# Kernel tuning notes

Measured on AMD Instinct MI355X. Metric: run time of the kernel, lower is better.

The kernel has to match this reference:

```python
import jax, jax.numpy as jnp
import numpy as np

EMBED, HIDDEN, VOCAB, FEAT_DIM = 256, 512, 10000, 1024
B, NREG, CAPLEN = 128, 49, 33


def setup_inputs() -> dict:
    key = jax.random.key(0)
    ks = jax.random.split(key, 20)
    xav = lambda k, shp: jax.random.uniform(k, shp, jnp.float32, -1.0, 1.0) * jnp.sqrt(6.0 / (shp[0] + shp[1]))
    d = {
        "features": jax.random.normal(ks[0], (B, NREG, FEAT_DIM), jnp.float32),
        "captions": jax.random.randint(ks[1], (B, CAPLEN), 0, VOCAB),
        "emb": jax.random.uniform(ks[2], (VOCAB, EMBED), jnp.float32, -0.1, 0.1),
        "W_ft": jax.random.uniform(ks[3], (EMBED, FEAT_DIM), jnp.float32, -0.1, 0.1),
        "b_ft": jnp.zeros((EMBED,), jnp.float32),
        "W_i": xav(ks[4], (2 * EMBED, HIDDEN)), "U_i": xav(ks[5], (HIDDEN, HIDDEN)), "b_i": jnp.zeros((HIDDEN,), jnp.float32),
        "W_f": xav(ks[6], (2 * EMBED, HIDDEN)), "U_f": xav(ks[7], (HIDDEN, HIDDEN)), "b_f": jnp.zeros((HIDDEN,), jnp.float32),
        "W_c": xav(ks[8], (2 * EMBED, HIDDEN)), "U_c": xav(ks[9], (HIDDEN, HIDDEN)), "b_c": jnp.zeros((HIDDEN,), jnp.float32),
        "W_o": xav(ks[10], (2 * EMBED, HIDDEN)), "U_o": xav(ks[11], (HIDDEN, HIDDEN)), "b_o": jnp.zeros((HIDDEN,), jnp.float32),
        "W_fc": jax.random.uniform(ks[12], (VOCAB, HIDDEN), jnp.float32, -0.1, 0.1),
        "b_fc": jnp.zeros((VOCAB,), jnp.float32),
    }
    return d


def reference(features, captions, emb, W_ft, b_ft,
              W_i, U_i, b_i, W_f, U_f, b_f, W_c, U_c, b_c, W_o, U_o, b_o,
              W_fc, b_fc):
    # mean-pool image regions, project to embed space
    feats_emb = features.mean(axis=1) @ W_ft.T + b_ft            # [B, E]
    embeds = emb[captions[:, :-1]]                                # [B, T, E]
    xs = jnp.swapaxes(embeds, 0, 1)                               # [T, B, E]

    h0 = jnp.zeros((features.shape[0], HIDDEN), features.dtype)
    c0 = jnp.zeros_like(h0)

    def step(carry, e_t):
        h, c = carry
        x = jnp.concatenate([e_t, feats_emb], axis=1)             # [B, 2E] (dropout=eval identity)
        i = jax.nn.sigmoid(x @ W_i + h @ U_i + b_i)
        f = jax.nn.sigmoid(x @ W_f + h @ U_f + b_f)
        g = jnp.tanh(x @ W_c + h @ U_c + b_c)
        o = jax.nn.sigmoid(x @ W_o + h @ U_o + b_o)
        c_new = f * c + i * g
        h_new = o * jnp.tanh(c_new)
        return (h_new, c_new), h_new

    _, hs = jax.lax.scan(step, (h0, c0), xs)                      # hs: [T, B, H]
    outputs = jnp.einsum('tbh,vh->btv', hs, W_fc) + b_fc          # [B, T, V]
    return outputs
```

## Files before the change

### kernel.cpp

```cpp
#include <hip/hip_runtime.h>
#include <hip/hip_bf16.h>

#define EMBED    256
#define HIDDEN   512
#define VOCAB    10000
#define WFC_PAD  10112
#define FEAT_DIM 1024
#define BATCH    128
#define NREGS    49
#define TSTEPS   32

typedef unsigned short u16;
typedef unsigned long long u64;
using f32x4 = __attribute__((ext_vector_type(4))) float;
using s16x8 = __attribute__((ext_vector_type(8))) short;
using u32x4 = __attribute__((ext_vector_type(4))) unsigned;

__device__ __forceinline__ u16 f2bf(float f) {
  __hip_bfloat16 h = __float2bfloat16(f);
  return *reinterpret_cast<u16*>(&h);
}
__device__ __forceinline__ float sig_(float x) {
  return 1.0f / (1.0f + __expf(-x));
}
__device__ __forceinline__ float tanh_(float x) {
  x = fminf(fmaxf(x, -15.f), 15.f);
  float e = __expf(2.f * x);
  return (e - 1.f) / (e + 1.f);
}
__device__ __forceinline__ void gl_lds16(const u16* g, u16* l) {
  __builtin_amdgcn_global_load_lds(
      (const __attribute__((address_space(1))) unsigned*)g,
      (__attribute__((address_space(3))) unsigned*)l, 16, 0, 0);
}

__global__ __launch_bounds__(256)
void k_feats(const float* __restrict__ features, const float* __restrict__ W_ft,
             const float* __restrict__ b_ft, float* __restrict__ feats_emb) {
  __shared__ float mean[FEAT_DIM];
  int b = blockIdx.x, tid = threadIdx.x;
  const float* fb = features + (size_t)b * NREGS * FEAT_DIM;
  for (int d = tid; d < FEAT_DIM; d += 256) {
    float s = 0.f;
    for (int r = 0; r < NREGS; ++r) s += fb[r * FEAT_DIM + d];
    mean[d] = s * (1.0f / 49.0f);
  }
  __syncthreads();
  const float* w = W_ft + (size_t)tid * FEAT_DIM;
  float acc = b_ft[tid];
#pragma unroll 4
  for (int d = 0; d < FEAT_DIM; d += 4) {
    float4 m4 = *(const float4*)&mean[d];
    float4 w4 = *(const float4*)&w[d];
    acc += m4.x * w4.x + m4.y * w4.y + m4.z * w4.z + m4.w * w4.w;
  }
  feats_emb[b * EMBED + tid] = acc;
}

struct GatePtrs {
  const float* W[4];
  const float* U[4];
  const float* b[4];
};

__global__ __launch_bounds__(256)
void k_transpose_wu(GatePtrs p, u16* __restrict__ WcatT, u16* __restrict__ UcatT) {
  __shared__ float tile[64][65];
  int g = blockIdx.y;
  const float* src = blockIdx.z ? p.U[g] : p.W[g];
  u16* dst = blockIdx.z ? UcatT : WcatT;
  int tj = (blockIdx.x & 7) * 64;
  int tk = (blockIdx.x >> 3) * 64;
  int tx = threadIdx.x & 63, ty = threadIdx.x >> 6;
#pragma unroll
  for (int i = 0; i < 16; ++i)
    tile[ty + 4 * i][tx] = src[(size_t)(tk + ty + 4 * i) * HIDDEN + tj + tx];
  __syncthreads();
#pragma unroll
  for (int i = 0; i < 16; ++i)
    dst[(size_t)(g * 512 + tj + ty + 4 * i) * 512 + tk + tx] = f2bf(tile[tx][ty + 4 * i]);
}

__global__ __launch_bounds__(256)
void k_prep2(GatePtrs p, const float* __restrict__ W_fc,
             float* __restrict__ bcat, u16* __restrict__ Wfc_bf) {
  int idx = blockIdx.x * 256 + threadIdx.x;
  if (idx < WFC_PAD * HIDDEN / 4) {
    size_t e0 = (size_t)idx * 4;
    ushort4 o;
    if (e0 < (size_t)VOCAB * HIDDEN) {
      float4 v = *(const float4*)(W_fc + e0);
      o.x = f2bf(v.x); o.y = f2bf(v.y); o.z = f2bf(v.z); o.w = f2bf(v.w);
    } else {
      o.x = o.y = o.z = o.w = 0;
    }
    *(ushort4*)(Wfc_bf + e0) = o;
  }
  if (idx < 4 * HIDDEN) bcat[idx] = p.b[idx >> 9][idx & 511];
}

__global__ __launch_bounds__(256)
void k_build_x(const float* __restrict__ emb, const int* __restrict__ captions,
               const float* __restrict__ feats_emb, u16* __restrict__ X) {
  int idx = blockIdx.x * 256 + threadIdx.x;
  int r = idx >> 9, col = idx & 511;
  int t = r >> 7, b = r & 127;
  float v;
  if (col < EMBED) {
    int tok = captions[b * 33 + t];
    v = emb[(size_t)tok * EMBED + col];
  } else {
    v = feats_emb[b * EMBED + (col - EMBED)];
  }
  X[idx] = f2bf(v);
}

__global__ __launch_bounds__(256)
void k_gemm_bt(const u16* __restrict__ A, const u16* __restrict__ Bt,
               const float* __restrict__ bias, float* __restrict__ C,
               int M, int N, int K, int out_mode) {
  __shared__ u16 Al[128 * 32];
  __shared__ u16 Bl[128 * 32];
  int tid = threadIdx.x;
  int lane = tid & 63;
  int w = tid >> 6;
  int wr = w & 1, wc = w >> 1;

  int Mtiles = gridDim.y, Ntiles = gridDim.x;
  int nwg = Mtiles * Ntiles;
  int id = blockIdx.y * Ntiles + blockIdx.x;
  int q = nwg >> 3, r = nwg & 7;
  int xcd = id & 7, pos = id >> 3;
  int wg = (xcd < r ? xcd * (q + 1) : r * (q + 1) + (xcd - r) * q) + pos;
  int m0 = (wg % Mtiles) * 128;
  int n0 = (wg / Mtiles) * 128;

  f32x4 acc[4][4];
#pragma unroll
  for (int i = 0; i < 4; ++i)
#pragma unroll
    for (int j = 0; j < 4; ++j) acc[i][j] = (f32x4){0.f, 0.f, 0.f, 0.f};

  int srowq = lane >> 2;
  int skq   = (lane & 3) * 8;

  for (int k0 = 0; k0 < K; k0 += 32) {
    __syncthreads();
#pragma unroll
    for (int i = 0; i < 2; ++i) {
      int rr = w * 32 + i * 16;
      gl_lds16(A + (size_t)(m0 + rr + srowq) * K + k0 + skq, Al + rr * 32);
      gl_lds16(Bt + (size_t)(n0 + rr + srowq) * K + k0 + skq, Bl + rr * 32);
    }
    __syncthreads();

    const u16* ab = Al + (wr * 64 + (lane & 15)) * 32 + (lane >> 4) * 8;
    const u16* bb = Bl + (wc * 64 + (lane & 15)) * 32 + (lane >> 4) * 8;
    s16x8 af[4], bf_[4];
#pragma unroll
    for (int mi = 0; mi < 4; ++mi) af[mi] = *(const s16x8*)(ab + mi * 16 * 32);
#pragma unroll
    for (int ni = 0; ni < 4; ++ni) bf_[ni] = *(const s16x8*)(bb + ni * 16 * 32);
#pragma unroll
    for (int mi = 0; mi < 4; ++mi)
#pragma unroll
      for (int ni = 0; ni < 4; ++ni)
        acc[mi][ni] = __builtin_amdgcn_mfma_f32_16x16x32_bf16(af[mi], bf_[ni], acc[mi][ni], 0, 0, 0);
  }

  int rbase = (lane >> 4) * 4;
  int colf = lane & 15;
#pragma unroll
  for (int mi = 0; mi < 4; ++mi) {
    int mbase = m0 + wr * 64 + mi * 16 + rbase;
#pragma unroll
    for (int ni = 0; ni < 4; ++ni) {
      int n = n0 + wc * 64 + ni * 16 + colf;
      if (n < N) {
        float bv = bias[n];
#pragma unroll
        for (int reg = 0; reg < 4; ++reg) {
          int mm = mbase + reg;
          float v = acc[mi][ni][reg] + bv;
          if (out_mode == 0) {
            C[(size_t)mm * N + n] = v;
          } else {
            C[(size_t)(mm & 127) * (TSTEPS * VOCAB) + (size_t)(mm >> 7) * VOCAB + n] = v;
          }
        }
      }
    }
  }
}

#define USTR 520

__global__ __launch_bounds__(256, 1)
void k_lstm_all(const u16* __restrict__ UcatT, const float* __restrict__ gates_pre,
                unsigned* __restrict__ hx, int* __restrict__ flags) {
  __shared__ u16 Ul[128 * USTR];
  int tid = threadIdx.x;
  int lane = tid & 63;
  int w = tid >> 6;
  int wr = w & 1, wj = w >> 1;
  int mg = blockIdx.x >> 4;
  int jb = blockIdx.x & 15;
  int b0 = mg * 32;
  int j0 = jb * 32;

  for (int i = tid; i < 128 * 64; i += 256) {
    int row = i >> 6;
    int kc = (i & 63) * 8;
    int gr = ((row >> 5) << 9) + j0 + (row & 31);
    uint4 v = *(const uint4*)(UcatT + (size_t)gr * 512 + kc);
    *(uint4*)(Ul + row * USTR + kc) = v;
  }
  __syncthreads();

  int jloc = wj * 16 + (lane & 15);
  int jj = j0 + jloc;
  int rb = wr * 16 + (lane >> 4) * 4;
  int arow = b0 + wr * 16 + (lane & 15);
  const u16* ubase = Ul + (size_t)jloc * USTR + (lane >> 4) * 8;
  int* myflag = flags + mg * 16 + jb;
  const int* pollp = flags + mg * 16 + (lane & 15);

  float c[4] = {0.f, 0.f, 0.f, 0.f};
  float gpv[16];

#pragma unroll
  for (int reg = 0; reg < 4; ++reg)
#pragma unroll
    for (int gi = 0; gi < 4; ++gi)
      gpv[reg * 4 + gi] = gates_pre[((size_t)(b0 + rb + reg)) * 2048 + gi * 512 + jj];

#pragma unroll 1
  for (int t = 0; t < TSTEPS; ++t) {
    f32x4 acc[4];
#pragma unroll
    for (int gi = 0; gi < 4; ++gi) acc[gi] = (f32x4){0.f, 0.f, 0.f, 0.f};

    if (t > 0) {
      int fv;
      do {
        asm volatile(
            "global_load_dword %0, %1, off sc0 sc1\n\t"
            "s_waitcnt vmcnt(0)"
            : "=v"(fv) : "v"(pollp) : "memory");
      } while (!__all(fv >= t));

      const u16* hp = (const u16*)hx + ((size_t)(t - 1) * 128 + arow) * 512 + (lane >> 4) * 8;
      u32x4 f[16];
      asm volatile(
          "global_load_dwordx4 %0, %4, off sc0 sc1\n\t"
          "global_load_dwordx4 %1, %4, off offset:64 sc0 sc1\n\t"
          "global_load_dwordx4 %2, %4, off offset:128 sc0 sc1\n\t"
          "global_load_dwordx4 %3, %4, off offset:192 sc0 sc1"
          : "=&v"(f[0]), "=&v"(f[1]), "=&v"(f[2]), "=&v"(f[3])
          : "v"(hp) : "memory");
      asm volatile(
          "global_load_dwordx4 %0, %4, off offset:256 sc0 sc1\n\t"
          "global_load_dwordx4 %1, %4, off offset:320 sc0 sc1\n\t"
          "global_load_dwordx4 %2, %4, off offset:384 sc0 sc1\n\t"
          "global_load_dwordx4 %3, %4, off offset:448 sc0 sc1"
          : "=&v"(f[4]), "=&v"(f[5]), "=&v"(f[6]), "=&v"(f[7])
          : "v"(hp) : "memory");
      asm volatile(
          "global_load_dwordx4 %0, %4, off offset:512 sc0 sc1\n\t"
          "global_load_dwordx4 %1, %4, off offset:576 sc0 sc1\n\t"
          "global_load_dwordx4 %2, %4, off offset:640 sc0 sc1\n\t"
          "global_load_dwordx4 %3, %4, off offset:704 sc0 sc1"
          : "=&v"(f[8]), "=&v"(f[9]), "=&v"(f[10]), "=&v"(f[11])
          : "v"(hp) : "memory");
      asm volatile(
          "global_load_dwordx4 %0, %4, off offset:768 sc0 sc1\n\t"
          "global_load_dwordx4 %1, %4, off offset:832 sc0 sc1\n\t"
          "global_load_dwordx4 %2, %4, off offset:896 sc0 sc1\n\t"
          "global_load_dwordx4 %3, %4, off offset:960 sc0 sc1\n\t"
          "s_waitcnt vmcnt(0)"
          : "=&v"(f[12]), "=&v"(f[13]), "=&v"(f[14]), "=&v"(f[15])
          : "v"(hp) : "memory");
      __builtin_amdgcn_sched_barrier(0);

#pragma unroll
      for (int kk = 0; kk < 16; ++kk) {
        s16x8 af = __builtin_bit_cast(s16x8, f[kk]);
#pragma unroll
        for (int gi = 0; gi < 4; ++gi) {
          s16x8 bf_ = *(const s16x8*)(ubase + (size_t)gi * 32 * USTR + kk * 32);
          acc[gi] = __builtin_amdgcn_mfma_f32_16x16x32_bf16(af, bf_, acc[gi], 0, 0, 0);
        }
      }
    }

#pragma unroll
    for (int reg = 0; reg < 4; ++reg) {
      float pi = acc[0][reg] + gpv[reg * 4 + 0];
      float pf = acc[1][reg] + gpv[reg * 4 + 1];
      float pg = acc[2][reg] + gpv[reg * 4 + 2];
      float po = acc[3][reg] + gpv[reg * 4 + 3];
      float iv = sig_(pi), fv = sig_(pf), gv = tanh_(pg), ov = sig_(po);
      float cn = fv * c[reg] + iv * gv;
      c[reg] = cn;
      float hn = ov * tanh_(cn);
      u16 hb = f2bf(hn);
      unsigned pv = hb;
      unsigned nv = __shfl_down(pv, 1);
      if ((lane & 1) == 0) {
        unsigned packed = pv | (nv << 16);
        unsigned* dst = hx + ((size_t)t * 128 + b0 + rb + reg) * 256 + (jj >> 1);
        asm volatile("global_store_dword %0, %1, off sc0 sc1"
                     :: "v"(dst), "v"(packed) : "memory");
      }
    }

    if (t < TSTEPS - 1) {
#pragma unroll
      for (int reg = 0; reg < 4; ++reg)
#pragma unroll
        for (int gi = 0; gi < 4; ++gi)
          gpv[reg * 4 + gi] =
              gates_pre[((size_t)(t + 1) * 128 + b0 + rb + reg) * 2048 + gi * 512 + jj];

      __syncthreads();
      if (tid == 0) {
        int fl = t + 1;
        asm volatile("global_store_dword %0, %1, off sc0 sc1"
                     :: "v"(myflag), "v"(fl) : "memory");
      }
    }
  }
}

extern "C" void kernel_launch(void* const* d_in, const int* in_sizes, int n_in,
                              void* d_out, int out_size, void* d_ws, size_t ws_size,
                              hipStream_t stream) {
  const float* features = (const float*)d_in[0];
  const int*   captions = (const int*)d_in[1];
  const float* emb      = (const float*)d_in[2];
  const float* W_ft     = (const float*)d_in[3];
  const float* b_ft     = (const float*)d_in[4];
  GatePtrs p;
  p.W[0] = (const float*)d_in[5];  p.U[0] = (const float*)d_in[6];  p.b[0] = (const float*)d_in[7];
  p.W[1] = (const float*)d_in[8];  p.U[1] = (const float*)d_in[9];  p.b[1] = (const float*)d_in[10];
  p.W[2] = (const float*)d_in[11]; p.U[2] = (const float*)d_in[12]; p.b[2] = (const float*)d_in[13];
  p.W[3] = (const float*)d_in[14]; p.U[3] = (const float*)d_in[15]; p.b[3] = (const float*)d_in[16];
  const float* W_fc = (const float*)d_in[17];
  const float* b_fc = (const float*)d_in[18];
  float* out = (float*)d_out;

  char* ws = (char*)d_ws;
  float*    feats_emb = (float*)(ws + 0);
  u16*      X         = (u16*)(ws + 131072);
  u16*      WcatT     = (u16*)(ws + 4325376);
  u16*      UcatT     = (u16*)(ws + 6422528);
  float*    bcat      = (float*)(ws + 8519680);
  u16*      Wfc_bf    = (u16*)(ws + 8527872);
  float*    gates_pre = (float*)(ws + 18882560);
  int*      flags     = (int*)(ws + 52436992);
  unsigned* hx        = (unsigned*)(ws + 52846592);

  hipMemsetAsync(flags, 0, 4 * 16 * sizeof(int), stream);

  k_feats<<<128, 256, 0, stream>>>(features, W_ft, b_ft, feats_emb);
  k_transpose_wu<<<dim3(64, 4, 2), 256, 0, stream>>>(p, WcatT, UcatT);
  k_prep2<<<(WFC_PAD * HIDDEN / 4 + 255) / 256, 256, 0, stream>>>(p, W_fc, bcat, Wfc_bf);
  k_build_x<<<(TSTEPS * BATCH * 2 * EMBED) / 256, 256, 0, stream>>>(emb, captions, feats_emb, X);

  k_gemm_bt<<<dim3(2048 / 128, 4096 / 128), 256, 0, stream>>>(
      X, WcatT, bcat, gates_pre, 4096, 2048, 512, 0);

  k_lstm_all<<<64, 256, 0, stream>>>(UcatT, gates_pre, hx, flags);

  k_gemm_bt<<<dim3(WFC_PAD / 128, 4096 / 128), 256, 0, stream>>>(
      (const u16*)hx, Wfc_bf, b_fc, out, 4096, VOCAB, 512, 1);
}
```

Before: 370.8 us.

## Fuse LSTM recurrence with vocab projection via ticketed persistent consumer blocks

Merges the LSTM recurrence kernel and the final vocab GEMM into one persistent launch. 64 blocks run the recurrence while the other 192 blocks grab (timestep, vocab-tile) tickets atomically, wait on the per-step flags, and compute the output projection for finished timesteps. The aim is to overlap the output GEMM with the serial recurrence and drop a kernel boundary. The costs are flag polling, the flag store now running on the last step too, and GEMM blocks competing with the recurrence blocks for memory bandwidth. The GEMM blocks could also stall the recurrence if the 64 LSTM blocks are not all co-resident.

```diff
diff --git a/kernel.cpp b/kernel.cpp
--- a/kernel.cpp
+++ b/kernel.cpp
@@ -5,6 +5,7 @@
 #define HIDDEN   512
 #define VOCAB    10000
 #define WFC_PAD  10112
+#define NTILES   79
 #define FEAT_DIM 1024
 #define BATCH    128
 #define NREGS    49
@@ -118,7 +119,7 @@
 __global__ __launch_bounds__(256)
 void k_gemm_bt(const u16* __restrict__ A, const u16* __restrict__ Bt,
                const float* __restrict__ bias, float* __restrict__ C,
-               int M, int N, int K, int out_mode) {
+               int M, int N, int K) {
   __shared__ u16 Al[128 * 32];
   __shared__ u16 Bl[128 * 32];
   int tid = threadIdx.x;
@@ -179,15 +180,8 @@
       if (n < N) {
         float bv = bias[n];
 #pragma unroll
-        for (int reg = 0; reg < 4; ++reg) {
-          int mm = mbase + reg;
-          float v = acc[mi][ni][reg] + bv;
-          if (out_mode == 0) {
-            C[(size_t)mm * N + n] = v;
-          } else {
-            C[(size_t)(mm & 127) * (TSTEPS * VOCAB) + (size_t)(mm >> 7) * VOCAB + n] = v;
-          }
-        }
+        for (int reg = 0; reg < 4; ++reg)
+          C[(size_t)(mbase + reg) * N + n] = acc[mi][ni][reg] + bv;
       }
     }
   }
@@ -196,137 +190,224 @@
 #define USTR 520
 
 __global__ __launch_bounds__(256, 1)
-void k_lstm_all(const u16* __restrict__ UcatT, const float* __restrict__ gates_pre,
-                unsigned* __restrict__ hx, int* __restrict__ flags) {
-  __shared__ u16 Ul[128 * USTR];
+void k_fused(const u16* __restrict__ UcatT, const float* __restrict__ gates_pre,
+             unsigned* __restrict__ hx, int* __restrict__ flags, int* __restrict__ ticket,
+             const u16* __restrict__ Wfc, const float* __restrict__ b_fc,
+             float* __restrict__ out) {
+  __shared__ u16 SH[128 * USTR];
+  __shared__ int tickLds;
   int tid = threadIdx.x;
   int lane = tid & 63;
   int w = tid >> 6;
-  int wr = w & 1, wj = w >> 1;
-  int mg = blockIdx.x >> 4;
-  int jb = blockIdx.x & 15;
-  int b0 = mg * 32;
-  int j0 = jb * 32;
-
-  for (int i = tid; i < 128 * 64; i += 256) {
-    int row = i >> 6;
-    int kc = (i & 63) * 8;
-    int gr = ((row >> 5) << 9) + j0 + (row & 31);
-    uint4 v = *(const uint4*)(UcatT + (size_t)gr * 512 + kc);
-    *(uint4*)(Ul + row * USTR + kc) = v;
-  }
-  __syncthreads();
-
-  int jloc = wj * 16 + (lane & 15);
-  int jj = j0 + jloc;
-  int rb = wr * 16 + (lane >> 4) * 4;
-  int arow = b0 + wr * 16 + (lane & 15);
-  const u16* ubase = Ul + (size_t)jloc * USTR + (lane >> 4) * 8;
-  int* myflag = flags + mg * 16 + jb;
-  const int* pollp = flags + mg * 16 + (lane & 15);
-
-  float c[4] = {0.f, 0.f, 0.f, 0.f};
-  float gpv[16];
-
-#pragma unroll
-  for (int reg = 0; reg < 4; ++reg)
-#pragma unroll
-    for (int gi = 0; gi < 4; ++gi)
-      gpv[reg * 4 + gi] = gates_pre[((size_t)(b0 + rb + reg)) * 2048 + gi * 512 + jj];
+
+  if (blockIdx.x < 64) {
+    u16* Ul = SH;
+    int wr = w & 1, wj = w >> 1;
+    int mg = blockIdx.x >> 4;
+    int jb = blockIdx.x & 15;
+    int b0 = mg * 32;
+    int j0 = jb * 32;
+
+    for (int i = tid; i < 128 * 64; i += 256) {
+      int row = i >> 6;
+      int kc = (i & 63) * 8;
+      int gr = ((row >> 5) << 9) + j0 + (row & 31);
+      uint4 v = *(const uint4*)(UcatT + (size_t)gr * 512 + kc);
+      *(uint4*)(Ul + row * USTR + kc) = v;
+    }
+    __syncthreads();
+
+    int jloc = wj * 16 + (lane & 15);
+    int jj = j0 + jloc;
+    int rb = wr * 16 + (lane >> 4) * 4;
+    int arow = b0 + wr * 16 + (lane & 15);
+    const u16* ubase = Ul + (size_t)jloc * USTR + (lane >> 4) * 8;
+    int* myflag = flags + mg * 16 + jb;
+    const int* pollp = flags + mg * 16 + (lane & 15);
+
+    float c[4] = {0.f, 0.f, 0.f, 0.f};
+    float gpv[16];
+
+#pragma unroll
+    for (int reg = 0; reg < 4; ++reg)
+#pragma unroll
+      for (int gi = 0; gi < 4; ++gi)
+        gpv[reg * 4 + gi] = gates_pre[((size_t)(b0 + rb + reg)) * 2048 + gi * 512 + jj];
 
 #pragma unroll 1
-  for (int t = 0; t < TSTEPS; ++t) {
-    f32x4 acc[4];
-#pragma unroll
-    for (int gi = 0; gi < 4; ++gi) acc[gi] = (f32x4){0.f, 0.f, 0.f, 0.f};
-
-    if (t > 0) {
-      int fv;
-      do {
+    for (int t = 0; t < TSTEPS; ++t) {
+      f32x4 acc[4];
+#pragma unroll
+      for (int gi = 0; gi < 4; ++gi) acc[gi] = (f32x4){0.f, 0.f, 0.f, 0.f};
+
+      if (t > 0) {
+        int fv;
+        do {
+          asm volatile(
+              "global_load_dword %0, %1, off sc0 sc1\n\t"
+              "s_waitcnt vmcnt(0)"
+              : "=v"(fv) : "v"(pollp) : "memory");
+        } while (!__all(fv >= t));
+
+        const u16* hp = (const u16*)hx + ((size_t)(t - 1) * 128 + arow) * 512 + (lane >> 4) * 8;
+        u32x4 f[16];
         asm volatile(
-            "global_load_dword %0, %1, off sc0 sc1\n\t"
+            "global_load_dwordx4 %0, %4, off sc0 sc1\n\t"
+            "global_load_dwordx4 %1, %4, off offset:64 sc0 sc1\n\t"
+            "global_load_dwordx4 %2, %4, off offset:128 sc0 sc1\n\t"
+            "global_load_dwordx4 %3, %4, off offset:192 sc0 sc1"
+            : "=&v"(f[0]), "=&v"(f[1]), "=&v"(f[2]), "=&v"(f[3])
+            : "v"(hp) : "memory");
+        asm volatile(
+            "global_load_dwordx4 %0, %4, off offset:256 sc0 sc1\n\t"
+            "global_load_dwordx4 %1, %4, off offset:320 sc0 sc1\n\t"
+            "global_load_dwordx4 %2, %4, off offset:384 sc0 sc1\n\t"
+            "global_load_dwordx4 %3, %4, off offset:448 sc0 sc1"
+            : "=&v"(f[4]), "=&v"(f[5]), "=&v"(f[6]), "=&v"(f[7])
+            : "v"(hp) : "memory");
+        asm volatile(
+            "global_load_dwordx4 %0, %4, off offset:512 sc0 sc1\n\t"
+            "global_load_dwordx4 %1, %4, off offset:576 sc0 sc1\n\t"
+            "global_load_dwordx4 %2, %4, off offset:640 sc0 sc1\n\t"
+            "global_load_dwordx4 %3, %4, off offset:704 sc0 sc1"
+            : "=&v"(f[8]), "=&v"(f[9]), "=&v"(f[10]), "=&v"(f[11])
+            : "v"(hp) : "memory");
+        asm volatile(
+            "global_load_dwordx4 %0, %4, off offset:768 sc0 sc1\n\t"
+            "global_load_dwordx4 %1, %4, off offset:832 sc0 sc1\n\t"
+            "global_load_dwordx4 %2, %4, off offset:896 sc0 sc1\n\t"
+            "global_load_dwordx4 %3, %4, off offset:960 sc0 sc1\n\t"
             "s_waitcnt vmcnt(0)"
-            : "=v"(fv) : "v"(pollp) : "memory");
-      } while (!__all(fv >= t));
-
-      const u16* hp = (const u16*)hx + ((size_t)(t - 1) * 128 + arow) * 512 + (lane >> 4) * 8;
-      u32x4 f[16];
-      asm volatile(
-          "global_load_dwordx4 %0, %4, off sc0 sc1\n\t"
-          "global_load_dwordx4 %1, %4, off offset:64 sc0 sc1\n\t"
-          "global_load_dwordx4 %2, %4, off offset:128 sc0 sc1\n\t"
-          "global_load_dwordx4 %3, %4, off offset:192 sc0 sc1"
-          : "=&v"(f[0]), "=&v"(f[1]), "=&v"(f[2]), "=&v"(f[3])
-          : "v"(hp) : "memory");
-      asm volatile(
-          "global_load_dwordx4 %0, %4, off offset:256 sc0 sc1\n\t"
-          "global_load_dwordx4 %1, %4, off offset:320 sc0 sc1\n\t"
-          "global_load_dwordx4 %2, %4, off offset:384 sc0 sc1\n\t"
-          "global_load_dwordx4 %3, %4, off offset:448 sc0 sc1"
-          : "=&v"(f[4]), "=&v"(f[5]), "=&v"(f[6]), "=&v"(f[7])
-          : "v"(hp) : "memory");
-      asm volatile(
-          "global_load_dwordx4 %0, %4, off offset:512 sc0 sc1\n\t"
-          "global_load_dwordx4 %1, %4, off offset:576 sc0 sc1\n\t"
-          "global_load_dwordx4 %2, %4, off offset:640 sc0 sc1\n\t"
-          "global_load_dwordx4 %3, %4, off offset:704 sc0 sc1"
-          : "=&v"(f[8]), "=&v"(f[9]), "=&v"(f[10]), "=&v"(f[11])
-          : "v"(hp) : "memory");
-      asm volatile(
-          "global_load_dwordx4 %0, %4, off offset:768 sc0 sc1\n\t"
-          "global_load_dwordx4 %1, %4, off offset:832 sc0 sc1\n\t"
-          "global_load_dwordx4 %2, %4, off offset:896 sc0 sc1\n\t"
-          "global_load_dwordx4 %3, %4, off offset:960 sc0 sc1\n\t"
-          "s_waitcnt vmcnt(0)"
-          : "=&v"(f[12]), "=&v"(f[13]), "=&v"(f[14]), "=&v"(f[15])
-          : "v"(hp) : "memory");
-      __builtin_amdgcn_sched_barrier(0);
-
-#pragma unroll
-      for (int kk = 0; kk < 16; ++kk) {
-        s16x8 af = __builtin_bit_cast(s16x8, f[kk]);
-#pragma unroll
-        for (int gi = 0; gi < 4; ++gi) {
-          s16x8 bf_ = *(const s16x8*)(ubase + (size_t)gi * 32 * USTR + kk * 32);
-          acc[gi] = __builtin_amdgcn_mfma_f32_16x16x32_bf16(af, bf_, acc[gi], 0, 0, 0);
+            : "=&v"(f[12]), "=&v"(f[13]), "=&v"(f[14]), "=&v"(f[15])
+            : "v"(hp) : "memory");
+        __builtin_amdgcn_sched_barrier(0);
+
+#pragma unroll
+        for (int kk = 0; kk < 16; ++kk) {
+          s16x8 af = __builtin_bit_cast(s16x8, f[kk]);
+#pragma unroll
+          for (int gi = 0; gi < 4; ++gi) {
+            s16x8 bf_ = *(const s16x8*)(ubase + (size_t)gi * 32 * USTR + kk * 32);
+            acc[gi] = __builtin_amdgcn_mfma_f32_16x16x32_bf16(af, bf_, acc[gi], 0, 0, 0);
+          }
         }
       }
-    }
-
-#pragma unroll
-    for (int reg = 0; reg < 4; ++reg) {
-      float pi = acc[0][reg] + gpv[reg * 4 + 0];
-      float pf = acc[1][reg] + gpv[reg * 4 + 1];
-      float pg = acc[2][reg] + gpv[reg * 4 + 2];
-      float po = acc[3][reg] + gpv[reg * 4 + 3];
-      float iv = sig_(pi), fv = sig_(pf), gv = tanh_(pg), ov = sig_(po);
-      float cn = fv * c[reg] + iv * gv;
-      c[reg] = cn;
-      float hn = ov * tanh_(cn);
-      u16 hb = f2bf(hn);
-      unsigned pv = hb;
-      unsigned nv = __shfl_down(pv, 1);
-      if ((lane & 1) == 0) {
-        unsigned packed = pv | (nv << 16);
-        unsigned* dst = hx + ((size_t)t * 128 + b0 + rb + reg) * 256 + (jj >> 1);
-        asm volatile("global_store_dword %0, %1, off sc0 sc1"
-                     :: "v"(dst), "v"(packed) : "memory");
-      }
-    }
-
-    if (t < TSTEPS - 1) {
-#pragma unroll
-      for (int reg = 0; reg < 4; ++reg)
-#pragma unroll
-        for (int gi = 0; gi < 4; ++gi)
-          gpv[reg * 4 + gi] =
-              gates_pre[((size_t)(t + 1) * 128 + b0 + rb + reg) * 2048 + gi * 512 + jj];
+
+#pragma unroll
+      for (int reg = 0; reg < 4; ++reg) {
+        float pi = acc[0][reg] + gpv[reg * 4 + 0];
+        float pf = acc[1][reg] + gpv[reg * 4 + 1];
+        float pg = acc[2][reg] + gpv[reg * 4 + 2];
+        float po = acc[3][reg] + gpv[reg * 4 + 3];
+        float iv = sig_(pi), fv2 = sig_(pf), gv = tanh_(pg), ov = sig_(po);
+        float cn = fv2 * c[reg] + iv * gv;
+        c[reg] = cn;
+        float hn = ov * tanh_(cn);
+        u16 hb = f2bf(hn);
+        unsigned pv = hb;
+        unsigned nv = __shfl_down(pv, 1);
+        if ((lane & 1) == 0) {
+          unsigned packed = pv | (nv << 16);
+          unsigned* dst = hx + ((size_t)t * 128 + b0 + rb + reg) * 256 + (jj >> 1);
+          asm volatile("global_store_dword %0, %1, off sc0 sc1"
+                       :: "v"(dst), "v"(packed) : "memory");
+        }
+      }
+
+      if (t < TSTEPS - 1) {
+#pragma unroll
+        for (int reg = 0; reg < 4; ++reg)
+#pragma unroll
+          for (int gi = 0; gi < 4; ++gi)
+            gpv[reg * 4 + gi] =
+                gates_pre[((size_t)(t + 1) * 128 + b0 + rb + reg) * 2048 + gi * 512 + jj];
+      }
 
       __syncthreads();
       if (tid == 0) {
         int fl = t + 1;
         asm volatile("global_store_dword %0, %1, off sc0 sc1"
                      :: "v"(myflag), "v"(fl) : "memory");
+      }
+    }
+  } else {
+    u16* Al = SH;
+    u16* Bl = SH + 128 * 32;
+    int wr = w & 1, wc = w >> 1;
+    int srowq = lane >> 2;
+    int skq   = (lane & 3) * 8;
+    const u16* hx16 = (const u16*)hx;
+
+    for (;;) {
+      if (tid == 0)
+        tickLds = __hip_atomic_fetch_add(ticket, 1, __ATOMIC_RELAXED, __HIP_MEMORY_SCOPE_AGENT);
+      __syncthreads();
+      int T = tickLds;
+      if (T >= TSTEPS * NTILES) break;
+      int t = T / NTILES, nt = T % NTILES;
+
+      {
+        const int* fp = flags + lane;
+        for (;;) {
+          int fv;
+          asm volatile(
+              "global_load_dword %0, %1, off sc0 sc1\n\t"
+              "s_waitcnt vmcnt(0)"
+              : "=v"(fv) : "v"(fp) : "memory");
+          if (__all(fv >= t + 1)) break;
+          __builtin_amdgcn_s_sleep(64);
+        }
+      }
+
+      const u16* A = hx16 + (size_t)t * 128 * 512;
+      int n0 = nt * 128;
+
+      f32x4 acc[4][4];
+#pragma unroll
+      for (int i = 0; i < 4; ++i)
+#pragma unroll
+        for (int j = 0; j < 4; ++j) acc[i][j] = (f32x4){0.f, 0.f, 0.f, 0.f};
+
+      for (int k0 = 0; k0 < HIDDEN; k0 += 32) {
+        __syncthreads();
+#pragma unroll
+        for (int i = 0; i < 2; ++i) {
+          int rr = w * 32 + i * 16;
+          gl_lds16(A + (size_t)(rr + srowq) * HIDDEN + k0 + skq, Al + rr * 32);
+          gl_lds16(Wfc + (size_t)(n0 + rr + srowq) * HIDDEN + k0 + skq, Bl + rr * 32);
+        }
+        __syncthreads();
+
+        const u16* ab = Al + (wr * 64 + (lane & 15)) * 32 + (lane >> 4) * 8;
+        const u16* bb = Bl + (wc * 64 + (lane & 15)) * 32 + (lane >> 4) * 8;
+        s16x8 af[4], bf_[4];
+#pragma unroll
+        for (int mi = 0; mi < 4; ++mi) af[mi] = *(const s16x8*)(ab + mi * 16 * 32);
+#pragma unroll
+        for (int ni = 0; ni < 4; ++ni) bf_[ni] = *(const s16x8*)(bb + ni * 16 * 32);
+#pragma unroll
+        for (int mi = 0; mi < 4; ++mi)
+#pragma unroll
+          for (int ni = 0; ni < 4; ++ni)
+            acc[mi][ni] = __builtin_amdgcn_mfma_f32_16x16x32_bf16(af[mi], bf_[ni], acc[mi][ni], 0, 0, 0);
+      }
+
+      int rbase = (lane >> 4) * 4;
+      int colf = lane & 15;
+#pragma unroll
+      for (int mi = 0; mi < 4; ++mi) {
+        int mbase = wr * 64 + mi * 16 + rbase;
+#pragma unroll
+        for (int ni = 0; ni < 4; ++ni) {
+          int n = n0 + wc * 64 + ni * 16 + colf;
+          if (n < VOCAB) {
+            float bv = b_fc[n];
+#pragma unroll
+            for (int reg = 0; reg < 4; ++reg)
+              out[(size_t)(mbase + reg) * (TSTEPS * VOCAB) + (size_t)t * VOCAB + n] =
+                  acc[mi][ni][reg] + bv;
+          }
+        }
       }
     }
   }
@@ -358,9 +439,10 @@
   u16*      Wfc_bf    = (u16*)(ws + 8527872);
   float*    gates_pre = (float*)(ws + 18882560);
   int*      flags     = (int*)(ws + 52436992);
+  int*      ticket    = flags + 64;
   unsigned* hx        = (unsigned*)(ws + 52846592);
 
-  hipMemsetAsync(flags, 0, 4 * 16 * sizeof(int), stream);
+  hipMemsetAsync(flags, 0, 512, stream);
 
   k_feats<<<128, 256, 0, stream>>>(features, W_ft, b_ft, feats_emb);
   k_transpose_wu<<<dim3(64, 4, 2), 256, 0, stream>>>(p, WcatT, UcatT);
@@ -368,10 +450,8 @@
   k_build_x<<<(TSTEPS * BATCH * 2 * EMBED) / 256, 256, 0, stream>>>(emb, captions, feats_emb, X);
 
   k_gemm_bt<<<dim3(2048 / 128, 4096 / 128), 256, 0, stream>>>(
-      X, WcatT, bcat, gates_pre, 4096, 2048, 512, 0);
-
-  k_lstm_all<<<64, 256, 0, stream>>>(UcatT, gates_pre, hx, flags);
-
-  k_gemm_bt<<<dim3(WFC_PAD / 128, 4096 / 128), 256, 0, stream>>>(
-      (const u16*)hx, Wfc_bf, b_fc, out, 4096, VOCAB, 512, 1);
-}
+      X, WcatT, bcat, gates_pre, 4096, 2048, 512);
+
+  k_fused<<<256, 256, 0, stream>>>(UcatT, gates_pre, hx, flags, ticket,
+                                   Wfc_bf, b_fc, out);
+}
```

Result: faster. 332.6 us (-10.3%).
